# Kernel tuning notes

Measured on AMD Instinct MI355X. Metric: run time of the kernel, lower is better.

## Reference

```python
import jax, jax.numpy as jnp
import numpy as np

EPS = 1e-5
NHEAD = 8
NEG = -1e9  # matches -inf masked-fill semantics; rows never fully masked after fallback


def layer_norm(x, g, b):
    m = jnp.mean(x, axis=-1, keepdims=True)
    v = jnp.var(x, axis=-1, keepdims=True)
    return (x - m) * jax.lax.rsqrt(v + EPS) * g + b


def mha(q, k, v, Wqkv, bqkv, Wo, bo, bias=None):
    # torch nn.MultiheadAttention math (batch_first). Wqkv: [C, 3C] (jax layout).
    B, N, C = q.shape
    M = k.shape[1]
    d = C // NHEAD
    Wq, Wk, Wv = jnp.split(Wqkv, 3, axis=1)
    bq, bk, bv = jnp.split(bqkv, 3)
    qp = (q @ Wq + bq).reshape(B, N, NHEAD, d)
    kp = (k @ Wk + bk).reshape(B, M, NHEAD, d)
    vp = (v @ Wv + bv).reshape(B, M, NHEAD, d)
    s = jnp.einsum('bnhd,bmhd->bhnm', qp, kp) / np.sqrt(d).astype(q.dtype)
    if bias is not None:
        s = s + bias  # [B,1,N,M] broadcast over heads
    a = jax.nn.softmax(s, axis=-1)
    o = jnp.einsum('bhnm,bmhd->bnhd', a, vp).reshape(B, N, C)
    return o @ Wo + bo


def setup_inputs() -> dict:
    key = jax.random.key(0)
    B, Nq, HW, C, F = 8, 100, 4096, 512, 2048
    ks = jax.random.split(key, 16)
    s = 0.02
    inp = {
        'q': jax.random.normal(ks[0], (B, Nq, C), jnp.float32),
        'kv': jax.random.normal(ks[1], (B, HW, C), jnp.float32),
        'mask_bin': jax.random.randint(ks[2], (B, Nq, HW), 0, 2, jnp.int32),
        # MaskedXAttn: attn params + norm_q/norm_kv
        'xa_Wqkv': jax.random.normal(ks[3], (C, 3 * C), jnp.float32) * s,
        'xa_bqkv': jnp.zeros((3 * C,), jnp.float32),
        'xa_Wo': jax.random.normal(ks[4], (C, C), jnp.float32) * s,
        'xa_bo': jnp.zeros((C,), jnp.float32),
        'xa_gq': jnp.ones((C,), jnp.float32),
        'xa_bq_ln': jnp.zeros((C,), jnp.float32),
        'xa_gkv': jnp.ones((C,), jnp.float32),
        'xa_bkv_ln': jnp.zeros((C,), jnp.float32),
        # self-attention
        'sa_Wqkv': jax.random.normal(ks[5], (C, 3 * C), jnp.float32) * s,
        'sa_bqkv': jnp.zeros((3 * C,), jnp.float32),
        'sa_Wo': jax.random.normal(ks[6], (C, C), jnp.float32) * s,
        'sa_bo': jnp.zeros((C,), jnp.float32),
        # norms
        'n1_g': jnp.ones((C,), jnp.float32), 'n1_b': jnp.zeros((C,), jnp.float32),
        'n2_g': jnp.ones((C,), jnp.float32), 'n2_b': jnp.zeros((C,), jnp.float32),
        # FFN (MLP with num_layers=2: Linear(C,F), ReLU, Linear(F,C))
        'ff_W1': jax.random.normal(ks[7], (C, F), jnp.float32) * s,
        'ff_b1': jnp.zeros((F,), jnp.float32),
        'ff_W2': jax.random.normal(ks[8], (F, C), jnp.float32) * s,
        'ff_b2': jnp.zeros((C,), jnp.float32),
    }
    return inp


def reference(q, kv, mask_bin,
              xa_Wqkv, xa_bqkv, xa_Wo, xa_bo, xa_gq, xa_bq_ln, xa_gkv, xa_bkv_ln,
              sa_Wqkv, sa_bqkv, sa_Wo, sa_bo,
              n1_g, n1_b, n2_g, n2_b,
              ff_W1, ff_b1, ff_W2, ff_b2):
    # --- masked cross-attention (vectorized equivalent of per-query loop) ---
    qn = layer_norm(q, xa_gq, xa_bq_ln)
    kvn = layer_norm(kv, xa_gkv, xa_bkv_ln)
    allow = mask_bin.astype(bool)                      # [B,Nq,HW] True = attend
    row_any = jnp.any(allow, axis=-1, keepdims=True)   # queries with empty mask -> full attention
    eff = jnp.where(row_any, allow, True)
    bias = jnp.where(eff, 0.0, NEG).astype(q.dtype)[:, None, :, :]  # [B,1,Nq,HW]
    xa = mha(qn, kvn, kvn, xa_Wqkv, xa_bqkv, xa_Wo, xa_bo, bias=bias)
    q = q + xa
    # --- self-attention over queries ---
    qn1 = layer_norm(q, n1_g, n1_b)
    sa = mha(qn1, qn1, qn1, sa_Wqkv, sa_bqkv, sa_Wo, sa_bo)
    q = q + sa
    # --- FFN ---
    qn2 = layer_norm(q, n2_g, n2_b)
    h = jax.nn.relu(qn2 @ ff_W1 + ff_b1)
    q = q + (h @ ff_W2 + ff_b2)
    return q
```

## Files before the change

### kernel.cpp

```cpp
#include <hip/hip_runtime.h>

typedef unsigned short u16;
typedef unsigned int u32;
typedef __bf16 bf16x8 __attribute__((ext_vector_type(8)));
typedef short s16x4 __attribute__((ext_vector_type(4)));
typedef float f32x4 __attribute__((ext_vector_type(4)));

#define NEG_INF -3.0e38f

__device__ __forceinline__ u16 f2bf(float f){
  union { float f; u32 u; } v; v.f = f;
  u32 r = v.u + 0x7fffu + ((v.u >> 16) & 1u);
  return (u16)(r >> 16);
}
__device__ __forceinline__ float bf2f(u16 h){
  union { u32 u; float f; } v; v.u = ((u32)h) << 16; return v.f;
}
__device__ __forceinline__ short f2bf_s(float f){
  union { __bf16 h; short s; } cv; cv.h = (__bf16)f; return cv.s;
}

__device__ __forceinline__ f32x4 mfma16(s16x4 a, s16x4 b, f32x4 c){
#if __has_builtin(__builtin_amdgcn_mfma_f32_16x16x16bf16_1k)
  return __builtin_amdgcn_mfma_f32_16x16x16bf16_1k(a, b, c, 0, 0, 0);
#else
  asm("v_mfma_f32_16x16x16_bf16 %0, %1, %2, %0" : "+v"(c) : "v"(a), "v"(b));
  return c;
#endif
}

__device__ __forceinline__ void gl_lds16(const void* g, void* l){
  __builtin_amdgcn_global_load_lds((const __attribute__((address_space(1))) void*)g,
      (__attribute__((address_space(3))) void*)l, 16, 0, 0);
}

__device__ __forceinline__ void ln_body(const float* __restrict__ xr,
    const float* __restrict__ g, const float* __restrict__ b,
    u16* __restrict__ orow, int lane){
  float4 v0 = *(const float4*)(xr + lane * 4);
  float4 v1 = *(const float4*)(xr + 256 + lane * 4);
  float s = v0.x+v0.y+v0.z+v0.w + v1.x+v1.y+v1.z+v1.w;
  float q = v0.x*v0.x+v0.y*v0.y+v0.z*v0.z+v0.w*v0.w
          + v1.x*v1.x+v1.y*v1.y+v1.z*v1.z+v1.w*v1.w;
  #pragma unroll
  for (int d=1; d<64; d<<=1){ s += __shfl_xor(s, d, 64); q += __shfl_xor(q, d, 64); }
  float mean = s * (1.0f/512.0f);
  float var  = q * (1.0f/512.0f) - mean*mean;
  float rs = rsqrtf(var + 1e-5f);
  float4 g0 = *(const float4*)(g + lane*4), g1 = *(const float4*)(g + 256 + lane*4);
  float4 b0 = *(const float4*)(b + lane*4), b1 = *(const float4*)(b + 256 + lane*4);
  uint2 pa, pb;
  pa.x = (u32)f2bf((v0.x-mean)*rs*g0.x + b0.x) | ((u32)f2bf((v0.y-mean)*rs*g0.y + b0.y) << 16);
  pa.y = (u32)f2bf((v0.z-mean)*rs*g0.z + b0.z) | ((u32)f2bf((v0.w-mean)*rs*g0.w + b0.w) << 16);
  pb.x = (u32)f2bf((v1.x-mean)*rs*g1.x + b1.x) | ((u32)f2bf((v1.y-mean)*rs*g1.y + b1.y) << 16);
  pb.y = (u32)f2bf((v1.z-mean)*rs*g1.z + b1.z) | ((u32)f2bf((v1.w-mean)*rs*g1.w + b1.w) << 16);
  *(uint2*)(orow + lane*4) = pa;
  *(uint2*)(orow + 256 + lane*4) = pb;
}

__global__ __launch_bounds__(256) void ln_rows(const float* __restrict__ x,
    const float* __restrict__ g, const float* __restrict__ b,
    u16* __restrict__ out, int rows){
  int wid = threadIdx.x >> 6, lane = threadIdx.x & 63;
  int row = blockIdx.x * 4 + wid;
  if (row >= rows) return;
  ln_body(x + (size_t)row*512, g, b, out + (size_t)row*512, lane);
}

__global__ __launch_bounds__(256) void ln_all(
    const float* __restrict__ x0, const float* __restrict__ g0, const float* __restrict__ b0,
    u16* __restrict__ o0, int nb0, int rows0,
    const float* __restrict__ x1, const float* __restrict__ g1, const float* __restrict__ b1,
    u16* __restrict__ o1, int rows1){
  int wid = threadIdx.x >> 6, lane = threadIdx.x & 63;
  int bb = blockIdx.x;
  if (bb < nb0){
    int row = bb*4 + wid;
    if (row >= rows0) return;
    ln_body(x0 + (size_t)row*512, g0, b0, o0 + (size_t)row*512, lane);
  } else {
    int row = (bb - nb0)*4 + wid;
    if (row >= rows1) return;
    ln_body(x1 + (size_t)row*512, g1, b1, o1 + (size_t)row*512, lane);
  }
}

__global__ __launch_bounds__(128) void mask_prep(const int* __restrict__ mask, u32* __restrict__ mw){
  int r = blockIdx.x;
  int t = threadIdx.x;
  const int* mr = mask + (size_t)r*4096 + t*32;
  u32 w = 0;
  #pragma unroll
  for (int j=0;j<32;j+=4){
    int4 v = *(const int4*)(mr + j);
    w |= (u32)(v.x!=0) << j;
    w |= (u32)(v.y!=0) << (j+1);
    w |= (u32)(v.z!=0) << (j+2);
    w |= (u32)(v.w!=0) << (j+3);
  }
  int any = __syncthreads_or((int)(w != 0));
  mw[(size_t)r*128 + t] = any ? w : 0xffffffffu;
}

struct WtJobs {
  const float* W[7]; u16* Wt[7];
  int K[7], Nfull[7], ncol0[7], nt[7], blk0[7];
};

__global__ __launch_bounds__(256) void wtrans_all(WtJobs J){
  __shared__ float tile[32][33];
  const float* W = J.W[0]; u16* Wt = J.Wt[0];
  int K = J.K[0], Nfull = J.Nfull[0], ncol0 = J.ncol0[0], nt = J.nt[0], blk0 = 0;
  #pragma unroll
  for (int i=1;i<7;i++)
    if ((int)blockIdx.x >= J.blk0[i]){
      W=J.W[i]; Wt=J.Wt[i]; K=J.K[i]; Nfull=J.Nfull[i]; ncol0=J.ncol0[i]; nt=J.nt[i]; blk0=J.blk0[i];
    }
  int lb = blockIdx.x - blk0;
  int tk = lb / nt, tn = lb % nt;
  int t = threadIdx.x;
  int col = t & 31, kr = t >> 5;
  #pragma unroll
  for (int i=0;i<4;i++){
    int k = tk*32 + kr + i*8;
    tile[kr + i*8][col] = W[(size_t)k*Nfull + ncol0 + tn*32 + col];
  }
  __syncthreads();
  int nl = t >> 3, kc = (t & 7) * 4;
  uint2 o;
  o.x = (u32)f2bf(tile[kc+0][nl]) | ((u32)f2bf(tile[kc+1][nl]) << 16);
  o.y = (u32)f2bf(tile[kc+2][nl]) | ((u32)f2bf(tile[kc+3][nl]) << 16);
  *(uint2*)(Wt + (size_t)(tn*32 + nl)*K + tk*32 + kc) = o;
}

template<int EPI>
__global__ __launch_bounds__(256) void gemm_bt(
    const u16* __restrict__ A, const u16* __restrict__ Bt, const float* __restrict__ bias,
    float* __restrict__ outf, u16* __restrict__ outb, const float* __restrict__ res,
    int Mrows, int N, int K, int scale_cols,
    int T1, int rows_per_b, int vstride, u16* __restrict__ out2, int swz)
{
  __shared__ __align__(16) u16 As[128*64];
  __shared__ __align__(16) u16 Bs[128*64];
  int bid = blockIdx.x;
  if (swz){ int cpx = gridDim.x >> 3; bid = (bid & 7)*cpx + (bid >> 3); }
  int NT = N >> 7;
  int mt = bid / NT, nt = bid % NT;
  int m0 = mt << 7, n0 = nt << 7;
  int tid = threadIdx.x;
  int wid = tid >> 6, lane = tid & 63;
  int wm = wid >> 1, wn = wid & 1;
  int lg = lane >> 4, l15 = lane & 15;

  f32x4 acc[4][4] = {};
  int ktiles = K >> 6;
  for (int kt = 0; kt < ktiles; ++kt){
    int k0 = kt << 6;
    if (kt) __syncthreads();
    #pragma unroll
    for (int i=0;i<4;i++){
      int L = i*4096 + tid*16;
      int T = L ^ (((L>>7)&7)<<4);
      int row = T >> 7, colb = T & 127;
      int ga = m0 + row; if (ga > Mrows-1) ga = Mrows-1;
      gl_lds16((const char*)A + ((size_t)ga*K + k0)*2 + colb, (char*)As + L);
    }
    #pragma unroll
    for (int i=0;i<4;i++){
      int L = i*4096 + tid*16;
      int T = L ^ (((L>>7)&7)<<4);
      int row = T >> 7, colb = T & 127;
      gl_lds16((const char*)Bt + ((size_t)(n0+row)*K + k0)*2 + colb, (char*)Bs + L);
    }
    __syncthreads();
    #pragma unroll
    for (int ks=0; ks<2; ++ks){
      bf16x8 af[4], bfr[4];
      #pragma unroll
      for (int mi=0; mi<4; ++mi){
        int r = wm*64 + mi*16 + l15;
        int byt = r*128 + ks*64 + lg*16;
        af[mi] = *(const bf16x8*)((const char*)As + (byt ^ ((r&7)<<4)));
      }
      #pragma unroll
      for (int ni=0; ni<4; ++ni){
        int r = wn*64 + ni*16 + l15;
        int byt = r*128 + ks*64 + lg*16;
        bfr[ni] = *(const bf16x8*)((const char*)Bs + (byt ^ ((r&7)<<4)));
      }
      __builtin_amdgcn_s_setprio(1);
      #pragma unroll
      for (int mi=0;mi<4;mi++)
        #pragma unroll
        for (int ni=0;ni<4;ni++)
          acc[mi][ni] = __builtin_amdgcn_mfma_f32_16x16x32_bf16(af[mi], bfr[ni], acc[mi][ni], 0,0,0);
      __builtin_amdgcn_s_setprio(0);
    }
  }

  float bv[4], scl[4];
  #pragma unroll
  for (int ni=0;ni<4;ni++){
    int c = n0 + wn*64 + ni*16 + l15;
    bv[ni]  = bias[c];
    scl[ni] = (c < scale_cols) ? 0.125f : 1.0f;
  }
  if (EPI == 3){
    #pragma unroll
    for (int ni=0;ni<4;ni++){
      int c = n0 + wn*64 + ni*16 + l15;
      #pragma unroll
      for (int mi=0;mi<4;mi++){
        int mr0 = m0 + wm*64 + mi*16 + lg*4;
        if (mr0 >= Mrows) continue;
        if (c < T1){
          #pragma unroll
          for (int r4=0;r4<4;r4++)
            outb[(size_t)(mr0+r4)*T1 + c] = f2bf((acc[mi][ni][r4] + bv[ni])*scl[ni]);
        } else {
          int bidx = mr0 / rows_per_b;
          int key  = mr0 - bidx*rows_per_b;
          uint2 o;
          o.x = (u32)f2bf(acc[mi][ni][0]+bv[ni]) | ((u32)f2bf(acc[mi][ni][1]+bv[ni])<<16);
          o.y = (u32)f2bf(acc[mi][ni][2]+bv[ni]) | ((u32)f2bf(acc[mi][ni][3]+bv[ni])<<16);
          *(uint2*)(out2 + ((size_t)bidx*512 + (c - T1))*vstride + key) = o;
        }
      }
    }
  } else {
    #pragma unroll
    for (int mi=0;mi<4;mi++){
      #pragma unroll
      for (int r4=0;r4<4;r4++){
        int m = m0 + wm*64 + mi*16 + lg*4 + r4;
        if (m >= Mrows) continue;
        #pragma unroll
        for (int ni=0;ni<4;ni++){
          int c = n0 + wn*64 + ni*16 + l15;
          float v = acc[mi][ni][r4] + bv[ni];
          if (EPI == 0){
            outb[(size_t)m*N + c] = f2bf(v*scl[ni]);
          } else if (EPI == 1){
            outb[(size_t)m*N + c] = f2bf(fmaxf(v, 0.0f));
          } else {
            outf[(size_t)m*N + c] = v + res[(size_t)m*N + c];
          }
        }
      }
    }
  }
}

template<bool PARTIAL>
__global__ __launch_bounds__(256) void attn_kernel(
    const u16* __restrict__ Qp, int ldq,
    const u16* __restrict__ Kp, int ldk, int kcol0,
    const u16* __restrict__ VT, int vld,
    const u32* __restrict__ maskw,
    float* __restrict__ pm, float* __restrict__ pl, u16* __restrict__ po,
    u16* __restrict__ o_out,
    int nq, int mk, int S, int H, int Bp, int swz)
{
  __shared__ __align__(16) u16 Ks[4*2048];
  __shared__ __align__(16) u16 Vs[4*2048];
  int bid = blockIdx.x;
  if (swz){ int cpx = gridDim.x >> 3; bid = (bid & 7)*cpx + (bid >> 3); }
  int s = bid % S; int h = (bid / S) % H; int b = bid / (S*H);
  int tid = threadIdx.x, wid = tid>>6, lane = tid&63;
  int lg = lane>>4, l15 = lane&15;
  int qbase = b*nq;

  bf16x8 qf[2][2];
  #pragma unroll
  for (int mt=0;mt<2;mt++){
    int qr = wid*32 + mt*16 + l15; int qc = qr < nq ? qr : nq-1;
    #pragma unroll
    for (int ks=0;ks<2;ks++)
      qf[mt][ks] = *(const bf16x8*)(Qp + (size_t)(qbase+qc)*ldq + h*64 + ks*32 + lg*8);
  }
  float m_r[2] = {NEG_INF, NEG_INF};
  float l_r[2] = {0.0f, 0.0f};
  f32x4 of[2][4] = {};

  int kps = mk / S;
  int kbeg = s * kps;
  int ntiles = (kps + 31) >> 5;
  int mwld = mk >> 5;

  auto stage = [&](int t, int bufi){
    int kb = kbeg + t*32;
    {
      int key = tid>>3, sst = tid&7;
      int seg = sst ^ (key&7);
      int kc = kb + key; if (kc > mk-1) kc = mk-1;
      const char* src = (const char*)(Kp + (size_t)(b*mk + kc)*ldk + kcol0 + h*64) + seg*16;
      gl_lds16(src, (char*)Ks + bufi*4096 + tid*16);
    }
    {
      int f = tid>>2, o16s = tid&3;
      int o16 = o16s ^ (f&3);
      const char* src = (const char*)(VT + ((size_t)b*512 + h*64 + f)*vld + kb) + o16*16;
      gl_lds16(src, (char*)Vs + bufi*4096 + tid*16);
    }
  };

  stage(0, 0);
  if (ntiles > 1) stage(1, 1);

  for (int t=0;t<ntiles;t++){
    if (t+2 < ntiles) stage(t+2, (t+2)&3);
    int pend = ((t+1<ntiles)?1:0) + ((t+2<ntiles)?1:0);
    if (pend==2)      asm volatile("s_waitcnt vmcnt(4)" ::: "memory");
    else if (pend==1) asm volatile("s_waitcnt vmcnt(2)" ::: "memory");
    else              asm volatile("s_waitcnt vmcnt(0)" ::: "memory");
    __builtin_amdgcn_s_barrier();

    const char* Kb = (const char*)Ks + (t&3)*4096;
    const char* Vb = (const char*)Vs + (t&3)*4096;
    int kb = kbeg + t*32;

    bf16x8 kf[2][2];
    #pragma unroll
    for (int nt2=0;nt2<2;nt2++)
      #pragma unroll
      for (int ks=0;ks<2;ks++)
        kf[nt2][ks] = *(const bf16x8*)(Kb + ((nt2*16+l15)<<7) + ((((ks<<2)+lg) ^ (l15&7))<<4));
    s16x4 vf[4][2];
    #pragma unroll
    for (int nf=0;nf<4;nf++)
      #pragma unroll
      for (int nt2=0;nt2<2;nt2++){
        int off8 = nt2*4+lg;
        vf[nf][nt2] = *(const s16x4*)(Vb + ((nf*16+l15)<<6)
                       + ((((off8>>1) ^ (l15&3))<<4)) + ((off8&1)<<3));
      }
    f32x4 sT[2][2] = {};
    #pragma unroll
    for (int ks=0;ks<2;ks++){
      __builtin_amdgcn_s_setprio(1);
      #pragma unroll
      for (int nt2=0;nt2<2;nt2++)
        #pragma unroll
        for (int mt=0;mt<2;mt++)
          sT[nt2][mt] = __builtin_amdgcn_mfma_f32_16x16x32_bf16(kf[nt2][ks], qf[mt][ks], sT[nt2][mt], 0,0,0);
      __builtin_amdgcn_s_setprio(0);
    }
    #pragma unroll
    for (int mt=0;mt<2;mt++){
      int qr = wid*32 + mt*16 + l15; int qc = qr < nq ? qr : nq-1;
      u32 w = maskw ? maskw[(size_t)(qbase+qc)*mwld + (kb>>5)] : 0xffffffffu;
      int krel = lg*4;
      float mx = NEG_INF;
      #pragma unroll
      for (int nt2=0;nt2<2;nt2++){
        u32 wb = w >> (nt2*16 + krel);
        #pragma unroll
        for (int r=0;r<4;r++){
          bool ok = ((wb>>r)&1u) && (kb + nt2*16 + krel + r < mk);
          float sv = ok ? sT[nt2][mt][r] : NEG_INF;
          sT[nt2][mt][r] = sv;
          mx = fmaxf(mx, sv);
        }
      }
      mx = fmaxf(mx, __shfl_xor(mx, 16, 64));
      mx = fmaxf(mx, __shfl_xor(mx, 32, 64));
      float mnew = fmaxf(m_r[mt], mx);
      float corr = __expf(m_r[mt] - mnew);
      m_r[mt] = mnew;
      float ps = 0.0f;
      s16x4 pb[2];
      #pragma unroll
      for (int nt2=0;nt2<2;nt2++){
        #pragma unroll
        for (int r=0;r<4;r++){
          float p = __expf(sT[nt2][mt][r] - mnew);
          ps += p;
          pb[nt2][r] = f2bf_s(p);
        }
      }
      ps += __shfl_xor(ps, 16, 64);
      ps += __shfl_xor(ps, 32, 64);
      l_r[mt] = l_r[mt]*corr + ps;
      #pragma unroll
      for (int nf=0;nf<4;nf++) of[mt][nf] *= corr;
      __builtin_amdgcn_s_setprio(1);
      #pragma unroll
      for (int nf=0;nf<4;nf++)
        #pragma unroll
        for (int nt2=0;nt2<2;nt2++)
          of[mt][nf] = mfma16(vf[nf][nt2], pb[nt2], of[mt][nf]);
      __builtin_amdgcn_s_setprio(0);
    }
    __builtin_amdgcn_s_barrier();
  }

  #pragma unroll
  for (int mt=0;mt<2;mt++){
    int q = wid*32 + mt*16 + l15;
    if (q < nq){
      if (PARTIAL){
        size_t base = (((size_t)(s*Bp + b)*H + h)*128 + q);
        if (lg == 0){ pm[base] = m_r[mt]; pl[base] = l_r[mt]; }
        #pragma unroll
        for (int nf=0;nf<4;nf++){
          uint2 o;
          o.x = (u32)f2bf(of[mt][nf][0]) | ((u32)f2bf(of[mt][nf][1])<<16);
          o.y = (u32)f2bf(of[mt][nf][2]) | ((u32)f2bf(of[mt][nf][3])<<16);
          *(uint2*)(po + base*64 + nf*16 + lg*4) = o;
        }
      } else {
        float inv = 1.0f / l_r[mt];
        #pragma unroll
        for (int nf=0;nf<4;nf++){
          uint2 o;
          o.x = (u32)f2bf(of[mt][nf][0]*inv) | ((u32)f2bf(of[mt][nf][1]*inv)<<16);
          o.y = (u32)f2bf(of[mt][nf][2]*inv) | ((u32)f2bf(of[mt][nf][3]*inv)<<16);
          *(uint2*)(o_out + (size_t)(qbase+q)*512 + h*64 + nf*16 + lg*4) = o;
        }
      }
    }
  }
}

__global__ __launch_bounds__(64) void attn_combine(
    const float* __restrict__ pm, const float* __restrict__ pl, const u16* __restrict__ po,
    u16* __restrict__ o_out, int S, int Bp, int H, int nq)
{
  int bid = blockIdx.x;
  int q = bid % nq; int h = (bid / nq) % H; int b = bid / (nq*H);
  int f = threadIdx.x;
  float mstar = NEG_INF;
  for (int s=0;s<S;s++){
    size_t idx = (((size_t)(s*Bp + b)*H + h)*128 + q);
    mstar = fmaxf(mstar, pm[idx]);
  }
  float L = 0.0f, acc = 0.0f;
  for (int s=0;s<S;s++){
    size_t idx = (((size_t)(s*Bp + b)*H + h)*128 + q);
    float w = __expf(pm[idx] - mstar);
    L += w * pl[idx];
    acc += w * bf2f(po[idx*64 + f]);
  }
  o_out[((size_t)b*nq + q)*512 + h*64 + f] = f2bf(acc / L);
}

extern "C" void kernel_launch(void* const* d_in, const int* in_sizes, int n_in,
                              void* d_out, int out_size, void* d_ws, size_t ws_size,
                              hipStream_t stream){
  const float* q_in    = (const float*)d_in[0];
  const float* kv_in   = (const float*)d_in[1];
  const int*   maskb   = (const int*)d_in[2];
  const float* xa_Wqkv = (const float*)d_in[3];
  const float* xa_bqkv = (const float*)d_in[4];
  const float* xa_Wo   = (const float*)d_in[5];
  const float* xa_bo   = (const float*)d_in[6];
  const float* xa_gq   = (const float*)d_in[7];
  const float* xa_bq   = (const float*)d_in[8];
  const float* xa_gkv  = (const float*)d_in[9];
  const float* xa_bkv  = (const float*)d_in[10];
  const float* sa_Wqkv = (const float*)d_in[11];
  const float* sa_bqkv = (const float*)d_in[12];
  const float* sa_Wo   = (const float*)d_in[13];
  const float* sa_bo   = (const float*)d_in[14];
  const float* n1_g = (const float*)d_in[15];
  const float* n1_b = (const float*)d_in[16];
  const float* n2_g = (const float*)d_in[17];
  const float* n2_b = (const float*)d_in[18];
  const float* ff_W1 = (const float*)d_in[19];
  const float* ff_b1 = (const float*)d_in[20];
  const float* ff_W2 = (const float*)d_in[21];
  const float* ff_b2 = (const float*)d_in[22];

  char* ws = (char*)d_ws;
  size_t off = 0;
  auto alloc = [&](size_t bytes)->char*{ char* p = ws + off; off = (off + bytes + 255) & ~(size_t)255; return p; };
  u16* wq  = (u16*)alloc((size_t)512*512*2);
  u16* wkv = (u16*)alloc((size_t)1024*512*2);
  u16* wsa = (u16*)alloc((size_t)1536*512*2);
  u16* wxo = (u16*)alloc((size_t)512*512*2);
  u16* wso = (u16*)alloc((size_t)512*512*2);
  u16* wf1 = (u16*)alloc((size_t)2048*512*2);
  u16* wf2 = (u16*)alloc((size_t)512*2048*2);
  u16* qn  = (u16*)alloc((size_t)800*512*2);
  u16* qp  = (u16*)alloc((size_t)800*512*2);
  u32* mw  = (u32*)alloc((size_t)800*128*4);
  u16* kp  = (u16*)alloc((size_t)32768*512*2);
  u16* vpT = (u16*)alloc((size_t)8*512*4096*2);
  size_t reuse_off = off;
  u16* kvn = (u16*)alloc((size_t)32768*512*2);
  size_t offB = reuse_off;
  auto allocB = [&](size_t bytes)->char*{ char* p = ws + offB; offB = (offB + bytes + 255) & ~(size_t)255; return p; };
  const int S = 16;
  float* pm   = (float*)allocB((size_t)S*64*128*4);
  float* pl   = (float*)allocB((size_t)S*64*128*4);
  u16*   po   = (u16*)allocB((size_t)S*64*128*64*2);
  u16* o_xa   = (u16*)allocB((size_t)800*512*2);
  float* x1   = (float*)allocB((size_t)800*512*4);
  u16* qn1    = (u16*)allocB((size_t)800*512*2);
  u16* saqkv  = (u16*)allocB((size_t)800*1024*2);
  u16* vTsa   = (u16*)allocB((size_t)8*512*128*2);
  u16* o_sa   = (u16*)allocB((size_t)800*512*2);
  float* x2   = (float*)allocB((size_t)800*512*4);
  u16* qn2    = (u16*)allocB((size_t)800*512*2);
  u16* hbuf   = (u16*)allocB((size_t)800*2048*2);

  WtJobs J;
  J.W[0]=xa_Wqkv; J.Wt[0]=wq;  J.K[0]=512;  J.Nfull[0]=1536; J.ncol0[0]=0;   J.nt[0]=16;
  J.W[1]=xa_Wqkv; J.Wt[1]=wkv; J.K[1]=512;  J.Nfull[1]=1536; J.ncol0[1]=512; J.nt[1]=32;
  J.W[2]=sa_Wqkv; J.Wt[2]=wsa; J.K[2]=512;  J.Nfull[2]=1536; J.ncol0[2]=0;   J.nt[2]=48;
  J.W[3]=xa_Wo;   J.Wt[3]=wxo; J.K[3]=512;  J.Nfull[3]=512;  J.ncol0[3]=0;   J.nt[3]=16;
  J.W[4]=sa_Wo;   J.Wt[4]=wso; J.K[4]=512;  J.Nfull[4]=512;  J.ncol0[4]=0;   J.nt[4]=16;
  J.W[5]=ff_W1;   J.Wt[5]=wf1; J.K[5]=512;  J.Nfull[5]=2048; J.ncol0[5]=0;   J.nt[5]=64;
  J.W[6]=ff_W2;   J.Wt[6]=wf2; J.K[6]=2048; J.Nfull[6]=512;  J.ncol0[6]=0;   J.nt[6]=16;
  int nblk[7];
  int tot = 0;
  for (int i=0;i<7;i++){ J.blk0[i] = tot; nblk[i] = (J.K[i]/32)*J.nt[i]; tot += nblk[i]; }
  wtrans_all<<<tot, 256, 0, stream>>>(J);

  ln_all<<<200+8192, 256, 0, stream>>>(q_in, xa_gq, xa_bq, qn, 200, 800,
                                       kv_in, xa_gkv, xa_bkv, kvn, 32768);
  mask_prep<<<800, 128, 0, stream>>>(maskb, mw);

  gemm_bt<0><<<7*4, 256, 0, stream>>>(qn, wq, xa_bqkv, nullptr, qp, nullptr,
                                      800, 512, 512, 512, 0, 1, 1, nullptr, 0);
  gemm_bt<3><<<256*8, 256, 0, stream>>>(kvn, wkv, xa_bqkv+512, nullptr, kp, nullptr,
                                        32768, 1024, 512, 0, 512, 4096, 4096, vpT, 1);
  attn_kernel<true><<<8*8*S, 256, 0, stream>>>(qp, 512, kp, 512, 0, vpT, 4096, mw,
                                               pm, pl, po, nullptr, 100, 4096, S, 8, 8, 1);
  attn_combine<<<8*8*100, 64, 0, stream>>>(pm, pl, po, o_xa, S, 8, 8, 100);
  gemm_bt<2><<<7*4, 256, 0, stream>>>(o_xa, wxo, xa_bo, x1, nullptr, q_in,
                                      800, 512, 512, 0, 0, 1, 1, nullptr, 0);
  ln_rows<<<200, 256, 0, stream>>>(x1, n1_g, n1_b, qn1, 800);
  hipMemsetAsync(vTsa, 0, (size_t)8*512*128*2, stream);
  gemm_bt<3><<<7*12, 256, 0, stream>>>(qn1, wsa, sa_bqkv, nullptr, saqkv, nullptr,
                                       800, 1536, 512, 512, 1024, 100, 128, vTsa, 0);
  attn_kernel<false><<<64, 256, 0, stream>>>(saqkv, 1024, saqkv, 1024, 512, vTsa, 128,
                                             nullptr, nullptr, nullptr, nullptr, o_sa,
                                             100, 100, 1, 8, 8, 0);
  gemm_bt<2><<<7*4, 256, 0, stream>>>(o_sa, wso, sa_bo, x2, nullptr, x1,
                                      800, 512, 512, 0, 0, 1, 1, nullptr, 0);
  ln_rows<<<200, 256, 0, stream>>>(x2, n2_g, n2_b, qn2, 800);
  gemm_bt<1><<<7*16, 256, 0, stream>>>(qn2, wf1, ff_b1, nullptr, hbuf, nullptr,
                                       800, 2048, 512, 0, 0, 1, 1, nullptr, 0);
  gemm_bt<2><<<7*4, 256, 0, stream>>>(hbuf, wf2, ff_b2, (float*)d_out, nullptr, x2,
                                      800, 512, 2048, 0, 0, 1, 1, nullptr, 0);
}
```

Baseline: 255.9 us.

## Compute V transposed directly via swapped-operand GEMM instead of scatter epilogue

```diff
diff --git a/kernel.cpp b/kernel.cpp
--- a/kernel.cpp
+++ b/kernel.cpp
@@ -137,8 +137,7 @@
 __global__ __launch_bounds__(256) void gemm_bt(
     const u16* __restrict__ A, const u16* __restrict__ Bt, const float* __restrict__ bias,
     float* __restrict__ outf, u16* __restrict__ outb, const float* __restrict__ res,
-    int Mrows, int N, int K, int scale_cols,
-    int T1, int rows_per_b, int vstride, u16* __restrict__ out2, int swz)
+    int Mrows, int N, int K, int scale_cols, int swz, int brmap)
 {
   __shared__ __align__(16) u16 As[128*64];
   __shared__ __align__(16) u16 Bs[128*64];
@@ -170,7 +169,9 @@
       int L = i*4096 + tid*16;
       int T = L ^ (((L>>7)&7)<<4);
       int row = T >> 7, colb = T & 127;
-      gl_lds16((const char*)Bt + ((size_t)(n0+row)*K + k0)*2 + colb, (char*)Bs + L);
+      int rowg = n0 + row;
+      if (brmap){ int rb = rowg & 127; rowg = (rowg>>7)*brmap + (rb < brmap ? rb : brmap-1); }
+      gl_lds16((const char*)Bt + ((size_t)rowg*K + k0)*2 + colb, (char*)Bs + L);
     }
     __syncthreads();
     #pragma unroll
@@ -198,36 +199,29 @@
     }
   }
 
-  float bv[4], scl[4];
-  #pragma unroll
-  for (int ni=0;ni<4;ni++){
-    int c = n0 + wn*64 + ni*16 + l15;
-    bv[ni]  = bias[c];
-    scl[ni] = (c < scale_cols) ? 0.125f : 1.0f;
-  }
-  if (EPI == 3){
+  if (EPI == 4){
+    #pragma unroll
+    for (int mi=0;mi<4;mi++){
+      #pragma unroll
+      for (int r4=0;r4<4;r4++){
+        int m = m0 + wm*64 + mi*16 + lg*4 + r4;
+        if (m >= Mrows) continue;
+        float rb = bias[m];
+        #pragma unroll
+        for (int ni=0;ni<4;ni++){
+          int c = n0 + wn*64 + ni*16 + l15;
+          outb[(size_t)m*N + c] = f2bf(acc[mi][ni][r4] + rb);
+        }
+      }
+    }
+  } else {
+    float bv[4], scl[4];
     #pragma unroll
     for (int ni=0;ni<4;ni++){
       int c = n0 + wn*64 + ni*16 + l15;
-      #pragma unroll
-      for (int mi=0;mi<4;mi++){
-        int mr0 = m0 + wm*64 + mi*16 + lg*4;
-        if (mr0 >= Mrows) continue;
-        if (c < T1){
-          #pragma unroll
-          for (int r4=0;r4<4;r4++)
-            outb[(size_t)(mr0+r4)*T1 + c] = f2bf((acc[mi][ni][r4] + bv[ni])*scl[ni]);
-        } else {
-          int bidx = mr0 / rows_per_b;
-          int key  = mr0 - bidx*rows_per_b;
-          uint2 o;
-          o.x = (u32)f2bf(acc[mi][ni][0]+bv[ni]) | ((u32)f2bf(acc[mi][ni][1]+bv[ni])<<16);
-          o.y = (u32)f2bf(acc[mi][ni][2]+bv[ni]) | ((u32)f2bf(acc[mi][ni][3]+bv[ni])<<16);
-          *(uint2*)(out2 + ((size_t)bidx*512 + (c - T1))*vstride + key) = o;
-        }
-      }
-    }
-  } else {
+      bv[ni]  = bias[c];
+      scl[ni] = (c < scale_cols) ? 0.125f : 1.0f;
+    }
     #pragma unroll
     for (int mi=0;mi<4;mi++){
       #pragma unroll
@@ -255,7 +249,7 @@
 __global__ __launch_bounds__(256) void attn_kernel(
     const u16* __restrict__ Qp, int ldq,
     const u16* __restrict__ Kp, int ldk, int kcol0,
-    const u16* __restrict__ VT, int vld,
+    const u16* __restrict__ VT, int vbs, int vfs,
     const u32* __restrict__ maskw,
     float* __restrict__ pm, float* __restrict__ pl, u16* __restrict__ po,
     u16* __restrict__ o_out,
@@ -299,7 +293,7 @@
     {
       int f = tid>>2, o16s = tid&3;
       int o16 = o16s ^ (f&3);
-      const char* src = (const char*)(VT + ((size_t)b*512 + h*64 + f)*vld + kb) + o16*16;
+      const char* src = (const char*)(VT + (size_t)b*vbs + (size_t)(h*64 + f)*vfs + kb) + o16*16;
       gl_lds16(src, (char*)Vs + bufi*4096 + tid*16);
     }
   };
@@ -485,7 +479,7 @@
   u16* qp  = (u16*)alloc((size_t)800*512*2);
   u32* mw  = (u32*)alloc((size_t)800*128*4);
   u16* kp  = (u16*)alloc((size_t)32768*512*2);
-  u16* vpT = (u16*)alloc((size_t)8*512*4096*2);
+  u16* vT2 = (u16*)alloc((size_t)512*32768*2 + 256);
   size_t reuse_off = off;
   u16* kvn = (u16*)alloc((size_t)32768*512*2);
   size_t offB = reuse_off;
@@ -498,7 +492,7 @@
   float* x1   = (float*)allocB((size_t)800*512*4);
   u16* qn1    = (u16*)allocB((size_t)800*512*2);
   u16* saqkv  = (u16*)allocB((size_t)800*1024*2);
-  u16* vTsa   = (u16*)allocB((size_t)8*512*128*2);
+  u16* vT2sa  = (u16*)allocB((size_t)512*1024*2);
   u16* o_sa   = (u16*)allocB((size_t)800*512*2);
   float* x2   = (float*)allocB((size_t)800*512*4);
   u16* qn2    = (u16*)allocB((size_t)800*512*2);
@@ -512,9 +506,8 @@
   J.W[4]=sa_Wo;   J.Wt[4]=wso; J.K[4]=512;  J.Nfull[4]=512;  J.ncol0[4]=0;   J.nt[4]=16;
   J.W[5]=ff_W1;   J.Wt[5]=wf1; J.K[5]=512;  J.Nfull[5]=2048; J.ncol0[5]=0;   J.nt[5]=64;
   J.W[6]=ff_W2;   J.Wt[6]=wf2; J.K[6]=2048; J.Nfull[6]=512;  J.ncol0[6]=0;   J.nt[6]=16;
-  int nblk[7];
   int tot = 0;
-  for (int i=0;i<7;i++){ J.blk0[i] = tot; nblk[i] = (J.K[i]/32)*J.nt[i]; tot += nblk[i]; }
+  for (int i=0;i<7;i++){ J.blk0[i] = tot; tot += (J.K[i]/32)*J.nt[i]; }
   wtrans_all<<<tot, 256, 0, stream>>>(J);
 
   ln_all<<<200+8192, 256, 0, stream>>>(q_in, xa_gq, xa_bq, qn, 200, 800,
@@ -522,26 +515,31 @@
   mask_prep<<<800, 128, 0, stream>>>(maskb, mw);
 
   gemm_bt<0><<<7*4, 256, 0, stream>>>(qn, wq, xa_bqkv, nullptr, qp, nullptr,
-                                      800, 512, 512, 512, 0, 1, 1, nullptr, 0);
-  gemm_bt<3><<<256*8, 256, 0, stream>>>(kvn, wkv, xa_bqkv+512, nullptr, kp, nullptr,
-                                        32768, 1024, 512, 0, 512, 4096, 4096, vpT, 1);
-  attn_kernel<true><<<8*8*S, 256, 0, stream>>>(qp, 512, kp, 512, 0, vpT, 4096, mw,
+                                      800, 512, 512, 512, 0, 0);
+  gemm_bt<0><<<256*4, 256, 0, stream>>>(kvn, wkv, xa_bqkv+512, nullptr, kp, nullptr,
+                                        32768, 512, 512, 0, 1, 0);
+  gemm_bt<4><<<4*256, 256, 0, stream>>>(wkv + (size_t)512*512, kvn, xa_bqkv+1024,
+                                        nullptr, vT2, nullptr,
+                                        512, 32768, 512, 0, 1, 0);
+  attn_kernel<true><<<8*8*S, 256, 0, stream>>>(qp, 512, kp, 512, 0, vT2, 4096, 32768, mw,
                                                pm, pl, po, nullptr, 100, 4096, S, 8, 8, 1);
   attn_combine<<<8*8*100, 64, 0, stream>>>(pm, pl, po, o_xa, S, 8, 8, 100);
   gemm_bt<2><<<7*4, 256, 0, stream>>>(o_xa, wxo, xa_bo, x1, nullptr, q_in,
-                                      800, 512, 512, 0, 0, 1, 1, nullptr, 0);
+                                      800, 512, 512, 0, 0, 0);
   ln_rows<<<200, 256, 0, stream>>>(x1, n1_g, n1_b, qn1, 800);
-  hipMemsetAsync(vTsa, 0, (size_t)8*512*128*2, stream);
-  gemm_bt<3><<<7*12, 256, 0, stream>>>(qn1, wsa, sa_bqkv, nullptr, saqkv, nullptr,
-                                       800, 1536, 512, 512, 1024, 100, 128, vTsa, 0);
-  attn_kernel<false><<<64, 256, 0, stream>>>(saqkv, 1024, saqkv, 1024, 512, vTsa, 128,
+  gemm_bt<0><<<7*8, 256, 0, stream>>>(qn1, wsa, sa_bqkv, nullptr, saqkv, nullptr,
+                                      800, 1024, 512, 512, 0, 0);
+  gemm_bt<4><<<4*8, 256, 0, stream>>>(wsa + (size_t)1024*512, qn1, sa_bqkv+1024,
+                                      nullptr, vT2sa, nullptr,
+                                      512, 1024, 512, 0, 0, 100);
+  attn_kernel<false><<<64, 256, 0, stream>>>(saqkv, 1024, saqkv, 1024, 512, vT2sa, 128, 1024,
                                              nullptr, nullptr, nullptr, nullptr, o_sa,
                                              100, 100, 1, 8, 8, 0);
   gemm_bt<2><<<7*4, 256, 0, stream>>>(o_sa, wso, sa_bo, x2, nullptr, x1,
-                                      800, 512, 512, 0, 0, 1, 1, nullptr, 0);
+                                      800, 512, 512, 0, 0, 0);
   ln_rows<<<200, 256, 0, stream>>>(x2, n2_g, n2_b, qn2, 800);
   gemm_bt<1><<<7*16, 256, 0, stream>>>(qn2, wf1, ff_b1, nullptr, hbuf, nullptr,
-                                       800, 2048, 512, 0, 0, 1, 1, nullptr, 0);
+                                       800, 2048, 512, 0, 0, 0);
   gemm_bt<2><<<7*4, 256, 0, stream>>>(hbuf, wf2, ff_b2, (float*)d_out, nullptr, x2,
-                                      800, 512, 2048, 0, 0, 1, 1, nullptr, 0);
-}
+                                      800, 512, 2048, 0, 0, 0);
+}
```

New measurement: 278.6 us. +8.9%, slower.
